# Kernel optimization log

Measured on AMD Instinct MI355X. Metric: run time of the kernel, lower is better.

Reference implementation:

```python
import jax, jax.numpy as jnp
import numpy as np

B, S, D, H = 2, 2048, 1024, 16


def setup_inputs() -> dict:
    key = jax.random.key(0)
    kq, kk, kv, kw = jax.random.split(key, 4)
    Q = jax.random.normal(kq, (B, S, D), dtype=jnp.float32)
    K = jax.random.normal(kk, (B, S, D), dtype=jnp.float32)
    V = jax.random.normal(kv, (B, S, D), dtype=jnp.float32)
    Wo = jax.random.normal(kw, (D, D), dtype=jnp.float32) * (1.0 / np.sqrt(D))
    return {"Q": Q, "K": K, "V": V, "Wo": Wo, "num_heads": H}


def reference(Q, K, V, Wo, num_heads):
    b, s, d = Q.shape
    dk = d // num_heads
    # split heads: [B,S,D] -> [B,H,S,dk]
    q = Q.reshape(b, s, num_heads, dk).transpose(0, 2, 1, 3)
    k = K.reshape(b, s, num_heads, dk).transpose(0, 2, 1, 3)
    v = V.reshape(b, s, num_heads, dk).transpose(0, 2, 1, 3)
    scale = 1.0 / jnp.sqrt(jnp.asarray(dk, dtype=q.dtype))
    logits = jnp.einsum('bhqd,bhkd->bhqk', q, k) * scale  # [B,H,S,S]
    probs = jax.nn.softmax(logits, axis=-1).astype(q.dtype)
    o = jnp.einsum('bhqk,bhkd->bhqd', probs, v)  # [B,H,S,dk]
    o = o.transpose(0, 2, 1, 3).reshape(b, s, d)  # concat heads
    # O = einsum('d dkh, ... dkh -> ... d', Wo, scores) == scores @ Wo^T
    return jnp.einsum('dk,bsk->bsd', Wo, o)
```

## Files before the change

kernel.cpp:

```cpp
#include <hip/hip_runtime.h>
#include <hip/hip_bf16.h>

#define B_ 2
#define S_ 2048
#define D_ 1024
#define H_ 16
#define DK_ 64

typedef __hip_bfloat16 bf16;
typedef short v8s __attribute__((ext_vector_type(8)));
typedef short v4s __attribute__((ext_vector_type(4)));
typedef float v4f __attribute__((ext_vector_type(4)));
typedef float v16f __attribute__((ext_vector_type(16)));
typedef int   v4i __attribute__((ext_vector_type(4)));

static __device__ __forceinline__ v16f mfma32(v8s a, v8s b, v16f c) {
  return __builtin_amdgcn_mfma_f32_32x32x16_bf16(a, b, c, 0, 0, 0);
}
static __device__ __forceinline__ void gl2lds16(const void* g, void* l) {
  __builtin_amdgcn_global_load_lds((const __attribute__((address_space(1))) void*)g,
                                   (__attribute__((address_space(3))) void*)l,
                                   16, 0, 0);
}
static __device__ __forceinline__ short f2bf(float x) {
  return (short)__builtin_bit_cast(unsigned short, __float2bfloat16(x));
}
static __device__ __forceinline__ int pk2f(float lo, float hi) {
  unsigned a = __builtin_bit_cast(unsigned, lo) + 0x8000u;
  unsigned b = __builtin_bit_cast(unsigned, hi) + 0x8000u;
  return (int)__builtin_amdgcn_perm(b, a, 0x07060302u);
}

__global__ __launch_bounds__(256) void cvt_k_kernel(const float* __restrict__ K,
                                                    bf16* __restrict__ Kb) {
  const int idx = blockIdx.x * 256 + threadIdx.x;
  const int seg = idx & 7;
  const int rest = idx >> 3;
  const int h = rest & 15;
  const int bs = rest >> 4;
  const float* src = K + (size_t)bs * D_ + h * 64 + seg * 8;
  v4f x = *(const v4f*)src, y = *(const v4f*)(src + 4);
  v8s r;
  r[0]=f2bf(x[0]); r[1]=f2bf(x[1]); r[2]=f2bf(x[2]); r[3]=f2bf(x[3]);
  r[4]=f2bf(y[0]); r[5]=f2bf(y[1]); r[6]=f2bf(y[2]); r[7]=f2bf(y[3]);
  const int b = bs >> 11, s = bs & 2047;
  *(v8s*)(Kb + ((size_t)(b * H_ + h) * S_ + s) * DK_ + seg * 8) = r;
}

__global__ __launch_bounds__(256) void tv_kernel(const float* __restrict__ V,
                                                 bf16* __restrict__ Vt) {
  __shared__ __align__(16) bf16 td[64 * 72];
  const int t = threadIdx.x;
  const int bh = blockIdx.x, b = bh >> 4, h = bh & 15;
  const int s0 = blockIdx.y * 64;
  const int srow = t >> 2;
  const int cs = t & 3;
  const float* vp = V + (size_t)(b * S_ + s0 + srow) * D_ + h * 64 + cs * 16;
#pragma unroll
  for (int j = 0; j < 4; j++) {
    v4f x = *(const v4f*)(vp + j * 4);
#pragma unroll
    for (int jj = 0; jj < 4; jj++)
      td[(cs * 16 + j * 4 + jj) * 72 + srow] = __float2bfloat16(x[jj]);
  }
  __syncthreads();
  const int d = t >> 2;
#pragma unroll
  for (int a2 = 0; a2 < 4; a2++) {
    const int pos = cs * 16 + a2 * 4;
    const int g = pos >> 5;
    const int a = (pos >> 2) & 7;
    const int kbase = g * 32 + ((a >> 2) << 4) + ((a & 1) << 3) + (((a >> 1) & 1) << 2);
    v4s val = *(const v4s*)(td + d * 72 + kbase);
    *(v4s*)(Vt + ((size_t)bh * DK_ + d) * S_ + s0 + pos) = val;
  }
}

__global__ __launch_bounds__(256) void cvt_wo_kernel(const float* __restrict__ Wo,
                                                     bf16* __restrict__ Wb) {
  const int i = (blockIdx.x * 256 + threadIdx.x) * 4;
  v4f a = *(const v4f*)(Wo + i);
  v4s r;
  r[0]=f2bf(a[0]); r[1]=f2bf(a[1]); r[2]=f2bf(a[2]); r[3]=f2bf(a[3]);
  *(v4s*)((short*)Wb + i) = r;
}

__global__ __launch_bounds__(256, 2) void attn3_kernel(
    const float* __restrict__ Q, const bf16* __restrict__ Kb,
    const bf16* __restrict__ Vt, bf16* __restrict__ Ow)
{
  __shared__ __align__(16) bf16 kk[2][64 * 64];
  __shared__ __align__(16) bf16 vv[2][64 * 64];
  __shared__ __align__(16) bf16 ep[4][32 * 72];

  const int t = threadIdx.x;
  const int w = t >> 6, l = t & 63, h2 = l >> 5, ln = l & 31;
  const int bh = blockIdx.x, b = bh >> 4, h = bh & 15;
  const int qbase = blockIdx.y * 128 + w * 32;

  const bf16* Kbh = Kb + (size_t)bh * (S_ * DK_);
  const bf16* Vbh = Vt + (size_t)bh * (DK_ * S_);

  const float sc = 0.18033688011112042f;
  v8s bq[4];
  {
    const float* qp = Q + ((size_t)b * S_ + qbase + ln) * D_ + h * DK_ + h2 * 8;
#pragma unroll
    for (int c = 0; c < 4; c++) {
      v4f x = *(const v4f*)(qp + c * 16);
      v4f y = *(const v4f*)(qp + c * 16 + 4);
      v4i r = { pk2f(x[0]*sc, x[1]*sc), pk2f(x[2]*sc, x[3]*sc),
                pk2f(y[0]*sc, y[1]*sc), pk2f(y[2]*sc, y[3]*sc) };
      bq[c] = __builtin_bit_cast(v8s, r);
    }
  }

  v16f accA, accB;
#pragma unroll
  for (int r = 0; r < 16; r++) { accA[r] = 0.f; accB[r] = 0.f; }
  float lpart = 0.f;

#pragma unroll
  for (int j = 0; j < 2; j++) {
    const int flat = j * 256 + t, row = flat >> 3, sp = flat & 7;
    gl2lds16(Kbh + (size_t)row * DK_ + ((sp ^ (row & 7)) * 8), &kk[0][flat * 8]);
    gl2lds16(Vbh + (size_t)row * S_ + ((sp ^ (row & 7)) * 8), &vv[0][flat * 8]);
  }

  int it = 0;
  for (int kb = 0; kb < S_; kb += 64, it ^= 1) {
    __syncthreads();
    if (kb + 64 < S_) {
#pragma unroll
      for (int j = 0; j < 2; j++) {
        const int flat = j * 256 + t, row = flat >> 3, sp = flat & 7;
        gl2lds16(Kbh + (size_t)(kb + 64 + row) * DK_ + ((sp ^ (row & 7)) * 8),
                 &kk[it ^ 1][flat * 8]);
        gl2lds16(Vbh + (size_t)row * S_ + (kb + 64) + ((sp ^ (row & 7)) * 8),
                 &vv[it ^ 1][flat * 8]);
      }
    }
    const bf16* kc_ = kk[it];
    const bf16* vc_ = vv[it];

    v16f s0, s1;
#pragma unroll
    for (int r = 0; r < 16; r++) { s0[r] = 0.f; s1[r] = 0.f; }
#pragma unroll
    for (int c = 0; c < 4; c++) {
      const int sd = 2 * c + h2;
      v8s a0 = *(const v8s*)(kc_ + ln * 64 + ((sd ^ (ln & 7)) * 8));
      v8s a1 = *(const v8s*)(kc_ + (32 + ln) * 64 + ((sd ^ (ln & 7)) * 8));
      s0 = mfma32(a0, bq[c], s0);
      s1 = mfma32(a1, bq[c], s1);
    }

    float p0[16], p1[16];
#pragma unroll
    for (int r = 0; r < 16; r++) { p0[r] = exp2f(s0[r]); p1[r] = exp2f(s1[r]); }
    float su = 0.f;
#pragma unroll
    for (int r = 0; r < 16; r++) su += p0[r] + p1[r];
    lpart += su;

    v4i i00 = { pk2f(p0[0],p0[1]),  pk2f(p0[2],p0[3]),  pk2f(p0[4],p0[5]),  pk2f(p0[6],p0[7]) };
    v4i i01 = { pk2f(p0[8],p0[9]),  pk2f(p0[10],p0[11]),pk2f(p0[12],p0[13]),pk2f(p0[14],p0[15]) };
    v4i i10 = { pk2f(p1[0],p1[1]),  pk2f(p1[2],p1[3]),  pk2f(p1[4],p1[5]),  pk2f(p1[6],p1[7]) };
    v4i i11 = { pk2f(p1[8],p1[9]),  pk2f(p1[10],p1[11]),pk2f(p1[12],p1[13]),pk2f(p1[14],p1[15]) };
    v8s pb00 = __builtin_bit_cast(v8s, i00);
    v8s pb01 = __builtin_bit_cast(v8s, i01);
    v8s pb10 = __builtin_bit_cast(v8s, i10);
    v8s pb11 = __builtin_bit_cast(v8s, i11);

#pragma unroll
    for (int st = 0; st < 2; st++) {
#pragma unroll
      for (int kc = 0; kc < 2; kc++) {
        const int q = st * 4 + kc * 2 + h2;
        v8s avA = *(const v8s*)(vc_ + ln * 64 + ((q ^ (ln & 7)) * 8));
        v8s avB = *(const v8s*)(vc_ + (32 + ln) * 64 + ((q ^ (ln & 7)) * 8));
        v8s pb = st ? (kc ? pb11 : pb10) : (kc ? pb01 : pb00);
        accA = mfma32(avA, pb, accA);
        accB = mfma32(avB, pb, accB);
      }
    }
  }

  const float lfull = lpart + __shfl_xor(lpart, 32);
  const float linv = 1.0f / lfull;
  bf16* epw = ep[w];
  const int swz = (ln >> 3) & 3;
#pragma unroll
  for (int r = 0; r < 16; r += 2) {
    const int off = (r & 3) + 4 * h2;
    const int spA = (r >> 2) ^ swz;
    const int vA = pk2f(accA[r] * linv, accA[r + 1] * linv);
    const int vB = pk2f(accB[r] * linv, accB[r + 1] * linv);
    *(int*)(epw + ln * 72 + spA * 8 + off) = vA;
    *(int*)(epw + ln * 72 + (4 + spA) * 8 + off) = vB;
  }
  __syncthreads();
#pragma unroll
  for (int i = 0; i < 4; i++) {
    const int flat = i * 64 + l;
    const int qr = flat >> 3, sd = flat & 7;
    const int pos = 4 * (sd >> 2) + ((sd & 3) ^ ((qr >> 3) & 3));
    v8s val = *(const v8s*)(epw + qr * 72 + pos * 8);
    *(v8s*)(Ow + ((size_t)b * S_ + qbase + qr) * D_ + h * DK_ + sd * 8) = val;
  }
}

__global__ __launch_bounds__(256, 4) void proj3_kernel(
    const bf16* __restrict__ A, const bf16* __restrict__ Wo, float* __restrict__ Out)
{
  __shared__ __align__(16) bf16 aa[2][64 * 64];
  __shared__ __align__(16) bf16 bb[2][64 * 64];

  const int t = threadIdx.x;
  const int w = t >> 6, l = t & 63, h2 = l >> 5, ln = l & 31;
  const int m0 = blockIdx.x * 64, n0 = blockIdx.y * 64;
  const int wm = (w & 1) * 32, wn = (w >> 1) * 32;

  v16f acc;
#pragma unroll
  for (int r = 0; r < 16; r++) acc[r] = 0.f;

#pragma unroll
  for (int j = 0; j < 2; j++) {
    const int flat = j * 256 + t, row = flat >> 3, sp = flat & 7;
    gl2lds16(A  + (size_t)(m0 + row) * D_ + ((sp ^ (row & 7)) * 8), &aa[0][flat * 8]);
    gl2lds16(Wo + (size_t)(n0 + row) * D_ + ((sp ^ (row & 7)) * 8), &bb[0][flat * 8]);
  }

  int it = 0;
  for (int k0 = 0; k0 < D_; k0 += 64, it ^= 1) {
    __syncthreads();
    if (k0 + 64 < D_) {
#pragma unroll
      for (int j = 0; j < 2; j++) {
        const int flat = j * 256 + t, row = flat >> 3, sp = flat & 7;
        gl2lds16(A  + (size_t)(m0 + row) * D_ + (k0 + 64) + ((sp ^ (row & 7)) * 8),
                 &aa[it ^ 1][flat * 8]);
        gl2lds16(Wo + (size_t)(n0 + row) * D_ + (k0 + 64) + ((sp ^ (row & 7)) * 8),
                 &bb[it ^ 1][flat * 8]);
      }
    }
    const bf16* ac = aa[it];
    const bf16* bc = bb[it];
#pragma unroll
    for (int c = 0; c < 4; c++) {
      const int sd = 2 * c + h2;
      v8s av = *(const v8s*)(ac + (wm + ln) * 64 + ((sd ^ (ln & 7)) * 8));
      v8s bv = *(const v8s*)(bc + (wn + ln) * 64 + ((sd ^ (ln & 7)) * 8));
      acc = mfma32(av, bv, acc);
    }
  }

#pragma unroll
  for (int r = 0; r < 16; r++) {
    const int row = m0 + wm + (r & 3) + 4 * h2 + 8 * (r >> 2);
    Out[(size_t)row * D_ + n0 + wn + ln] = acc[r];
  }
}

extern "C" void kernel_launch(void* const* d_in, const int* in_sizes, int n_in,
                              void* d_out, int out_size, void* d_ws, size_t ws_size,
                              hipStream_t stream) {
  (void)in_sizes; (void)n_in; (void)out_size; (void)ws_size;
  const float* Q  = (const float*)d_in[0];
  const float* K  = (const float*)d_in[1];
  const float* V  = (const float*)d_in[2];
  const float* Wo = (const float*)d_in[3];
  float* out = (float*)d_out;

  bf16* kb   = (bf16*)d_ws;
  bf16* vt   = kb + (size_t)4 * 1024 * 1024;
  bf16* ows  = vt + (size_t)4 * 1024 * 1024;
  bf16* wo_b = ows + (size_t)4 * 1024 * 1024;

  cvt_k_kernel <<<dim3(2048),   256, 0, stream>>>(K, kb);
  tv_kernel    <<<dim3(32, 32), 256, 0, stream>>>(V, vt);
  cvt_wo_kernel<<<dim3(1024),   256, 0, stream>>>(Wo, wo_b);
  attn3_kernel <<<dim3(32, 16), 256, 0, stream>>>(Q, kb, vt, ows);
  proj3_kernel <<<dim3(64, 16), 256, 0, stream>>>(ows, wo_b, out);
}
```

Baseline: 178.1 us.

## Split attention over two key halves, merge partials, and fuse preprocessing kernels

The attention kernel now splits the key/value range in two along a new grid dimension. Each half writes a normalized bf16 partial output plus its softmax denominator, and a new merge kernel combines the halves weighted by their denominators. This doubles the number of blocks (512 to 1024) and raises the launch-bounds occupancy hint, to fill more of the device; the epilogue staging also reuses the K tile LDS instead of a separate buffer. The three K/V/Wo conversion kernels are folded into one launch to cut launch overhead. In exchange it adds extra global traffic for the partial outputs and the merge pass, plus one more rounding of the output to bf16.

Result: no change. 176.8 us (-0.7%).

```diff
diff --git a/kernel.cpp b/kernel.cpp
--- a/kernel.cpp
+++ b/kernel.cpp
@@ -13,6 +13,7 @@
 typedef float v4f __attribute__((ext_vector_type(4)));
 typedef float v16f __attribute__((ext_vector_type(16)));
 typedef int   v4i __attribute__((ext_vector_type(4)));
+typedef int   v2i __attribute__((ext_vector_type(2)));
 
 static __device__ __forceinline__ v16f mfma32(v8s a, v8s b, v16f c) {
   return __builtin_amdgcn_mfma_f32_32x32x16_bf16(a, b, c, 0, 0, 0);
@@ -30,73 +31,80 @@
   unsigned b = __builtin_bit_cast(unsigned, hi) + 0x8000u;
   return (int)__builtin_amdgcn_perm(b, a, 0x07060302u);
 }
-
-__global__ __launch_bounds__(256) void cvt_k_kernel(const float* __restrict__ K,
-                                                    bf16* __restrict__ Kb) {
-  const int idx = blockIdx.x * 256 + threadIdx.x;
-  const int seg = idx & 7;
-  const int rest = idx >> 3;
-  const int h = rest & 15;
-  const int bs = rest >> 4;
-  const float* src = K + (size_t)bs * D_ + h * 64 + seg * 8;
-  v4f x = *(const v4f*)src, y = *(const v4f*)(src + 4);
-  v8s r;
-  r[0]=f2bf(x[0]); r[1]=f2bf(x[1]); r[2]=f2bf(x[2]); r[3]=f2bf(x[3]);
-  r[4]=f2bf(y[0]); r[5]=f2bf(y[1]); r[6]=f2bf(y[2]); r[7]=f2bf(y[3]);
-  const int b = bs >> 11, s = bs & 2047;
-  *(v8s*)(Kb + ((size_t)(b * H_ + h) * S_ + s) * DK_ + seg * 8) = r;
-}
-
-__global__ __launch_bounds__(256) void tv_kernel(const float* __restrict__ V,
-                                                 bf16* __restrict__ Vt) {
+static __device__ __forceinline__ float bf2f(short s) {
+  return __builtin_bit_cast(float, ((unsigned)(unsigned short)s) << 16);
+}
+
+__global__ __launch_bounds__(256) void pre_kernel(
+    const float* __restrict__ K, const float* __restrict__ V,
+    const float* __restrict__ Wo, bf16* __restrict__ Kb,
+    bf16* __restrict__ Vt, bf16* __restrict__ Wb)
+{
   __shared__ __align__(16) bf16 td[64 * 72];
   const int t = threadIdx.x;
-  const int bh = blockIdx.x, b = bh >> 4, h = bh & 15;
-  const int s0 = blockIdx.y * 64;
-  const int srow = t >> 2;
-  const int cs = t & 3;
-  const float* vp = V + (size_t)(b * S_ + s0 + srow) * D_ + h * 64 + cs * 16;
-#pragma unroll
-  for (int j = 0; j < 4; j++) {
-    v4f x = *(const v4f*)(vp + j * 4);
-#pragma unroll
-    for (int jj = 0; jj < 4; jj++)
-      td[(cs * 16 + j * 4 + jj) * 72 + srow] = __float2bfloat16(x[jj]);
-  }
-  __syncthreads();
-  const int d = t >> 2;
-#pragma unroll
-  for (int a2 = 0; a2 < 4; a2++) {
-    const int pos = cs * 16 + a2 * 4;
-    const int g = pos >> 5;
-    const int a = (pos >> 2) & 7;
-    const int kbase = g * 32 + ((a >> 2) << 4) + ((a & 1) << 3) + (((a >> 1) & 1) << 2);
-    v4s val = *(const v4s*)(td + d * 72 + kbase);
-    *(v4s*)(Vt + ((size_t)bh * DK_ + d) * S_ + s0 + pos) = val;
-  }
-}
-
-__global__ __launch_bounds__(256) void cvt_wo_kernel(const float* __restrict__ Wo,
-                                                     bf16* __restrict__ Wb) {
-  const int i = (blockIdx.x * 256 + threadIdx.x) * 4;
-  v4f a = *(const v4f*)(Wo + i);
-  v4s r;
-  r[0]=f2bf(a[0]); r[1]=f2bf(a[1]); r[2]=f2bf(a[2]); r[3]=f2bf(a[3]);
-  *(v4s*)((short*)Wb + i) = r;
-}
-
-__global__ __launch_bounds__(256, 2) void attn3_kernel(
+  const int bx = blockIdx.x;
+
+  if (bx < 2048) {
+    const int idx = bx * 256 + t;
+    const int seg = idx & 7;
+    const int rest = idx >> 3;
+    const int h = rest & 15;
+    const int bs = rest >> 4;
+    const float* src = K + (size_t)bs * D_ + h * 64 + seg * 8;
+    v4f x = *(const v4f*)src, y = *(const v4f*)(src + 4);
+    v8s r;
+    r[0]=f2bf(x[0]); r[1]=f2bf(x[1]); r[2]=f2bf(x[2]); r[3]=f2bf(x[3]);
+    r[4]=f2bf(y[0]); r[5]=f2bf(y[1]); r[6]=f2bf(y[2]); r[7]=f2bf(y[3]);
+    const int b = bs >> 11, s = bs & 2047;
+    *(v8s*)(Kb + ((size_t)(b * H_ + h) * S_ + s) * DK_ + seg * 8) = r;
+  } else if (bx < 3072) {
+    const int idx = bx - 2048;
+    const int bh = idx >> 5, b = bh >> 4, h = bh & 15;
+    const int s0 = (idx & 31) * 64;
+    const int srow = t >> 2;
+    const int cs = t & 3;
+    const float* vp = V + (size_t)(b * S_ + s0 + srow) * D_ + h * 64 + cs * 16;
+#pragma unroll
+    for (int j = 0; j < 4; j++) {
+      v4f x = *(const v4f*)(vp + j * 4);
+#pragma unroll
+      for (int jj = 0; jj < 4; jj++)
+        td[(cs * 16 + j * 4 + jj) * 72 + srow] = __float2bfloat16(x[jj]);
+    }
+    __syncthreads();
+    const int d = t >> 2;
+#pragma unroll
+    for (int a2 = 0; a2 < 4; a2++) {
+      const int pos = cs * 16 + a2 * 4;
+      const int g = pos >> 5;
+      const int a = (pos >> 2) & 7;
+      const int kbase = g * 32 + ((a >> 2) << 4) + ((a & 1) << 3) + (((a >> 1) & 1) << 2);
+      v4s val = *(const v4s*)(td + d * 72 + kbase);
+      *(v4s*)(Vt + ((size_t)bh * DK_ + d) * S_ + s0 + pos) = val;
+    }
+  } else {
+    const int i = ((bx - 3072) * 256 + t) * 4;
+    v4f a = *(const v4f*)(Wo + i);
+    v4s r;
+    r[0]=f2bf(a[0]); r[1]=f2bf(a[1]); r[2]=f2bf(a[2]); r[3]=f2bf(a[3]);
+    *(v4s*)((short*)Wb + i) = r;
+  }
+}
+
+__global__ __launch_bounds__(256, 4) void attn4_kernel(
     const float* __restrict__ Q, const bf16* __restrict__ Kb,
-    const bf16* __restrict__ Vt, bf16* __restrict__ Ow)
+    const bf16* __restrict__ Vt, bf16* __restrict__ Op0,
+    bf16* __restrict__ Op1, float* __restrict__ Lp)
 {
   __shared__ __align__(16) bf16 kk[2][64 * 64];
   __shared__ __align__(16) bf16 vv[2][64 * 64];
-  __shared__ __align__(16) bf16 ep[4][32 * 72];
 
   const int t = threadIdx.x;
   const int w = t >> 6, l = t & 63, h2 = l >> 5, ln = l & 31;
   const int bh = blockIdx.x, b = bh >> 4, h = bh & 15;
   const int qbase = blockIdx.y * 128 + w * 32;
+  const int z = blockIdx.z;
+  const int kb0 = z << 10;
 
   const bf16* Kbh = Kb + (size_t)bh * (S_ * DK_);
   const bf16* Vbh = Vt + (size_t)bh * (DK_ * S_);
@@ -123,14 +131,14 @@
 #pragma unroll
   for (int j = 0; j < 2; j++) {
     const int flat = j * 256 + t, row = flat >> 3, sp = flat & 7;
-    gl2lds16(Kbh + (size_t)row * DK_ + ((sp ^ (row & 7)) * 8), &kk[0][flat * 8]);
-    gl2lds16(Vbh + (size_t)row * S_ + ((sp ^ (row & 7)) * 8), &vv[0][flat * 8]);
+    gl2lds16(Kbh + (size_t)(kb0 + row) * DK_ + ((sp ^ (row & 7)) * 8), &kk[0][flat * 8]);
+    gl2lds16(Vbh + (size_t)row * S_ + kb0 + ((sp ^ (row & 7)) * 8), &vv[0][flat * 8]);
   }
 
   int it = 0;
-  for (int kb = 0; kb < S_; kb += 64, it ^= 1) {
+  for (int kb = kb0; kb < kb0 + 1024; kb += 64, it ^= 1) {
     __syncthreads();
-    if (kb + 64 < S_) {
+    if (kb + 64 < kb0 + 1024) {
 #pragma unroll
       for (int j = 0; j < 2; j++) {
         const int flat = j * 256 + t, row = flat >> 3, sp = flat & 7;
@@ -186,28 +194,61 @@
     }
   }
 
+  __syncthreads();
   const float lfull = lpart + __shfl_xor(lpart, 32);
   const float linv = 1.0f / lfull;
-  bf16* epw = ep[w];
-  const int swz = (ln >> 3) & 3;
-#pragma unroll
-  for (int r = 0; r < 16; r += 2) {
-    const int off = (r & 3) + 4 * h2;
-    const int spA = (r >> 2) ^ swz;
-    const int vA = pk2f(accA[r] * linv, accA[r + 1] * linv);
-    const int vB = pk2f(accB[r] * linv, accB[r + 1] * linv);
-    *(int*)(epw + ln * 72 + spA * 8 + off) = vA;
-    *(int*)(epw + ln * 72 + (4 + spA) * 8 + off) = vB;
-  }
-  __syncthreads();
+  bf16* epw = &kk[0][0] + w * 2048;
+#pragma unroll
+  for (int r = 0; r < 16; r += 4) {
+    const int off = 4 * h2;
+    const int sgA = (r >> 2) ^ (ln & 3);
+    const int sgB = 4 + sgA;
+    v2i pa = { pk2f(accA[r]*linv,   accA[r+1]*linv),
+               pk2f(accA[r+2]*linv, accA[r+3]*linv) };
+    v2i pb = { pk2f(accB[r]*linv,   accB[r+1]*linv),
+               pk2f(accB[r+2]*linv, accB[r+3]*linv) };
+    *(v2i*)(epw + ln * 64 + sgA * 8 + off) = pa;
+    *(v2i*)(epw + ln * 64 + sgB * 8 + off) = pb;
+  }
+  if (h2 == 0)
+    Lp[((size_t)z * 32 + bh) * S_ + qbase + ln] = lfull;
+
+  bf16* Op = z ? Op1 : Op0;
 #pragma unroll
   for (int i = 0; i < 4; i++) {
     const int flat = i * 64 + l;
     const int qr = flat >> 3, sd = flat & 7;
-    const int pos = 4 * (sd >> 2) + ((sd & 3) ^ ((qr >> 3) & 3));
-    v8s val = *(const v8s*)(epw + qr * 72 + pos * 8);
-    *(v8s*)(Ow + ((size_t)b * S_ + qbase + qr) * D_ + h * DK_ + sd * 8) = val;
-  }
+    const int phys = ((sd & 3) ^ (qr & 3)) | (sd & 4);
+    v8s val = *(const v8s*)(epw - w * 2048 + (w * 32 + qr) * 64 + phys * 8);
+    *(v8s*)(Op + ((size_t)b * S_ + qbase - w * 32 + w * 32 + qr) * D_ + h * DK_ + sd * 8) = val;
+  }
+}
+
+__global__ __launch_bounds__(256) void merge_kernel(
+    const bf16* __restrict__ Op0, const bf16* __restrict__ Op1,
+    const float* __restrict__ Lp, bf16* __restrict__ O)
+{
+  const int flat = blockIdx.x * 256 + threadIdx.x;
+  const int qrow = flat >> 7;
+  const int seg = flat & 127;
+  const int b = qrow >> 11, s = qrow & 2047;
+  const int h = seg >> 3;
+  const int bh = b * H_ + h;
+  const float l0 = Lp[(size_t)bh * S_ + s];
+  const float l1 = Lp[(size_t)(32 + bh) * S_ + s];
+  const float inv = 1.0f / (l0 + l1);
+  const float w0 = l0 * inv, w1 = l1 * inv;
+  const size_t off = (size_t)qrow * D_ + seg * 8;
+  v8s a = *(const v8s*)(Op0 + off);
+  v8s c = *(const v8s*)(Op1 + off);
+  v4i r;
+#pragma unroll
+  for (int j = 0; j < 4; j++) {
+    float lo = w0 * bf2f(a[2*j])   + w1 * bf2f(c[2*j]);
+    float hi = w0 * bf2f(a[2*j+1]) + w1 * bf2f(c[2*j+1]);
+    r[j] = pk2f(lo, hi);
+  }
+  *(v8s*)(O + off) = __builtin_bit_cast(v8s, r);
 }
 
 __global__ __launch_bounds__(256, 4) void proj3_kernel(
@@ -273,14 +314,17 @@
   const float* Wo = (const float*)d_in[3];
   float* out = (float*)d_out;
 
-  bf16* kb   = (bf16*)d_ws;
-  bf16* vt   = kb + (size_t)4 * 1024 * 1024;
-  bf16* ows  = vt + (size_t)4 * 1024 * 1024;
-  bf16* wo_b = ows + (size_t)4 * 1024 * 1024;
-
-  cvt_k_kernel <<<dim3(2048),   256, 0, stream>>>(K, kb);
-  tv_kernel    <<<dim3(32, 32), 256, 0, stream>>>(V, vt);
-  cvt_wo_kernel<<<dim3(1024),   256, 0, stream>>>(Wo, wo_b);
-  attn3_kernel <<<dim3(32, 16), 256, 0, stream>>>(Q, kb, vt, ows);
-  proj3_kernel <<<dim3(64, 16), 256, 0, stream>>>(ows, wo_b, out);
-}
+  bf16* base = (bf16*)d_ws;
+  bf16* kb   = base;
+  bf16* vt   = base + (size_t)4  * 1024 * 1024;
+  bf16* wo_b = base + (size_t)8  * 1024 * 1024;
+  bf16* op0  = base + (size_t)9  * 1024 * 1024;
+  bf16* op1  = base + (size_t)13 * 1024 * 1024;
+  float* lp  = (float*)(base + (size_t)17 * 1024 * 1024);
+  bf16* ows  = kb;
+
+  pre_kernel  <<<dim3(4096),       256, 0, stream>>>(K, V, Wo, kb, vt, wo_b);
+  attn4_kernel<<<dim3(32, 16, 2),  256, 0, stream>>>(Q, kb, vt, op0, op1, lp);
+  merge_kernel<<<dim3(2048),       256, 0, stream>>>(op0, op1, lp, ows);
+  proj3_kernel<<<dim3(64, 16),     256, 0, stream>>>(ows, wo_b, out);
+}
```
